# Kernel tuning notes

Hardware: AMD Instinct MI355X
Metric: run time of the kernel (lower is better)

## Reference

```python
import jax, jax.numpy as jnp
import numpy as np
import math

B, S, HID = 1, 4096, 2048
H, KVH, D = 32, 8, 64
N_REP = H // KVH  # 4


def _rope(x, cos, sin):
    # x: [B, h, S, D]; cos/sin: [S, D//2]
    x2 = x.reshape(*x.shape[:-1], D // 2, 2)
    x0, x1 = x2[..., 0], x2[..., 1]
    c = cos[None, None, :, :]
    s = sin[None, None, :, :]
    # complex multiply (x0 + i x1) * (c + i s)
    o0 = x0 * c - x1 * s
    o1 = x0 * s + x1 * c
    return jnp.stack([o0, o1], axis=-1).reshape(x.shape)


def setup_inputs() -> dict:
    key = jax.random.key(0)
    ks = jax.random.split(key, 6)
    hidden_states = jax.random.normal(ks[0], (B, S, 2 * HID), dtype=jnp.float32)
    scale = 0.02
    wq = jax.random.normal(ks[1], (H * D, 2 * HID), dtype=jnp.float32) * scale
    wk = jax.random.normal(ks[2], (KVH * D, 2 * HID), dtype=jnp.float32) * scale
    wv = jax.random.normal(ks[3], (KVH * D, 2 * HID), dtype=jnp.float32) * scale
    wo = jax.random.normal(ks[4], (HID, H * D), dtype=jnp.float32) * scale
    # standard RoPE frequencies (theta=10000), shape [S, D//2]
    inv_freq = 1.0 / (10000.0 ** (np.arange(0, D, 2, dtype=np.float32) / D))
    angles = np.arange(S, dtype=np.float32)[:, None] * inv_freq[None, :]
    freqs_cos = jnp.asarray(np.cos(angles), dtype=jnp.float32)
    freqs_sin = jnp.asarray(np.sin(angles), dtype=jnp.float32)
    return {"hidden_states": hidden_states, "wq": wq, "wk": wk, "wv": wv,
            "wo": wo, "freqs_cos": freqs_cos, "freqs_sin": freqs_sin}


def reference(hidden_states, wq, wk, wv, wo, freqs_cos, freqs_sin):
    bsz, q_len, _ = hidden_states.shape
    q = (hidden_states @ wq.T).reshape(bsz, q_len, H, D).transpose(0, 2, 1, 3)   # [B,H,S,D]
    k = (hidden_states @ wk.T).reshape(bsz, q_len, KVH, D).transpose(0, 2, 1, 3)  # [B,KVH,S,D]
    v = (hidden_states @ wv.T).reshape(bsz, q_len, KVH, D).transpose(0, 2, 1, 3)
    q = _rope(q, freqs_cos, freqs_sin)
    k = _rope(k, freqs_cos, freqs_sin)
    # GQA repeat_kv
    k = jnp.repeat(k, N_REP, axis=1)  # [B,H,S,D]
    v = jnp.repeat(v, N_REP, axis=1)
    scores = jnp.einsum('bhqd,bhkd->bhqk', q, k) / math.sqrt(D)  # [B,H,S,S]
    weights = jax.nn.softmax(scores.astype(jnp.float32), axis=-1).astype(q.dtype)
    attn = jnp.einsum('bhqk,bhkd->bhqd', weights, v)  # [B,H,S,D]
    attn = attn.transpose(0, 2, 1, 3).reshape(bsz, q_len, H * D)
    return attn @ wo.T  # [B,S,HID]
```

## Files before the change

kernel.cpp:

```cpp
#include <hip/hip_runtime.h>
#include <hip/hip_bf16.h>

typedef __attribute__((ext_vector_type(4))) float f32x4;
typedef __attribute__((ext_vector_type(8))) __bf16 bf16x8;
typedef __attribute__((ext_vector_type(8))) short short8;
typedef __attribute__((ext_vector_type(4))) short short4v;
typedef __attribute__((ext_vector_type(2))) unsigned int uint2v;

#define SEQ 4096
#define NQKV 3072

static __device__ __forceinline__ unsigned short f2bf(float x) {
  unsigned int u = __float_as_uint(x);
  u += 0x7fffu + ((u >> 16) & 1u);
  return (unsigned short)(u >> 16);
}
static __device__ __forceinline__ float bf2f(unsigned short b) {
  return __uint_as_float(((unsigned int)b) << 16);
}
static __device__ __forceinline__ unsigned int cvtpk_bf16(float lo, float hi) {
  unsigned int r;
  asm("v_cvt_pk_bf16_f32 %0, %1, %2" : "=v"(r) : "v"(lo), "v"(hi));
  return r;
}
static __device__ __forceinline__ float exp2_fast(float x) {
  float r;
  asm("v_exp_f32 %0, %1" : "=v"(r) : "v"(x));
  return r;
}

__global__ void cvt_f32_bf16(const float* __restrict__ src,
                             unsigned short* __restrict__ dst, int n4) {
  int i = blockIdx.x * blockDim.x + threadIdx.x;
  if (i >= n4) return;
  f32x4 v = ((const f32x4*)src)[i];
  short4v o;
#pragma unroll
  for (int j = 0; j < 4; ++j) o[j] = (short)f2bf(v[j]);
  ((short4v*)dst)[i] = o;
}

template <int BN, bool OUT_F32>
__global__ __launch_bounds__(512, 2) void gemm256(const unsigned short* __restrict__ A,
                                                  const unsigned short* __restrict__ Bt,
                                                  void* __restrict__ Cp,
                                                  int M, int N, int K) {
  constexpr int NJ = BN / 64;
  constexpr int TC = 16 + BN / 16;
  constexpr int SPW = (TC + 7) / 8;
  constexpr int DUP = 8 * SPW - TC;

  __shared__ unsigned short AbL[3][8192];
  __shared__ unsigned short BbL[3][BN * 32];

  const int t512 = threadIdx.x;
  const int l = t512 & 63;
  const int wid = t512 >> 6;
  const int wm = wid >> 2, wn = wid & 3;
  const int lr = l & 15, lg = l >> 4;
  const int m0 = blockIdx.y * 256, n0 = blockIdx.x * BN;

  const int lrow = l >> 2;
  const int scb = ((l & 3) << 4) ^ ((lrow & 3) << 4);

  const int rswz = (lr & 3) << 4;

  f32x4 acc[8][NJ];
#pragma unroll
  for (int i = 0; i < 8; ++i)
#pragma unroll
    for (int j = 0; j < NJ; ++j) acc[i][j] = (f32x4){0.f, 0.f, 0.f, 0.f};

  auto stage = [&](int buf, int t) {
    const int kt = t * 32;
#pragma unroll
    for (int s = 0; s < SPW; ++s) {
      int id = wid * SPW + s;
      if (DUP > 0 && id >= TC) id -= DUP;
      if (id < 16) {
        const char* src = (const char*)(A + (size_t)(m0 + id * 16 + lrow) * K + kt) + scb;
        __builtin_amdgcn_global_load_lds(
            (const __attribute__((address_space(1))) void*)src,
            (__attribute__((address_space(3))) void*)&AbL[buf][id * 512], 16, 0, 0);
      } else {
        const int b = id - 16;
        const char* src = (const char*)(Bt + (size_t)(n0 + b * 16 + lrow) * K + kt) + scb;
        __builtin_amdgcn_global_load_lds(
            (const __attribute__((address_space(1))) void*)src,
            (__attribute__((address_space(3))) void*)&BbL[buf][b * 512], 16, 0, 0);
      }
    }
  };

  const int NT = K / 32;

  stage(0, 0);
  stage(1, 1);
  if constexpr (SPW == 4) asm volatile("s_waitcnt vmcnt(4)" ::: "memory");
  else                    asm volatile("s_waitcnt vmcnt(3)" ::: "memory");
  __builtin_amdgcn_s_barrier();
  __builtin_amdgcn_sched_barrier(0);

  int cur = 0;
  for (int t = 0; t < NT; ++t) {
    int pf = cur + 2; if (pf >= 3) pf -= 3;
    if (t + 2 < NT) stage(pf, t + 2);

    const char* Ab0 = (const char*)&AbL[cur][0] + (size_t)(wm * 128 + lr) * 64;
    const char* Bb0 = (const char*)&BbL[cur][0] + (size_t)(wn * (BN / 4) + lr) * 64;
    bf16x8 af[8], bfv[NJ];
#pragma unroll
    for (int i = 0; i < 8; ++i)
      af[i] = *(const bf16x8*)(Ab0 + i * 1024 + ((lg * 16) ^ rswz));
#pragma unroll
    for (int j = 0; j < NJ; ++j)
      bfv[j] = *(const bf16x8*)(Bb0 + j * 1024 + ((lg * 16) ^ rswz));

    asm volatile("s_waitcnt lgkmcnt(0)" ::: "memory");
    __builtin_amdgcn_sched_barrier(0);

    __builtin_amdgcn_s_setprio(1);
#pragma unroll
    for (int i = 0; i < 8; ++i)
#pragma unroll
      for (int j = 0; j < NJ; ++j)
        acc[i][j] = __builtin_amdgcn_mfma_f32_16x16x32_bf16(af[i], bfv[j], acc[i][j], 0, 0, 0);
    __builtin_amdgcn_s_setprio(0);

    if (t + 2 < NT) {
      if constexpr (SPW == 4) asm volatile("s_waitcnt vmcnt(4)" ::: "memory");
      else                    asm volatile("s_waitcnt vmcnt(3)" ::: "memory");
    } else if (t + 1 < NT) {
      asm volatile("s_waitcnt vmcnt(0)" ::: "memory");
    }
    if (t + 1 < NT) {
      __builtin_amdgcn_s_barrier();
      __builtin_amdgcn_sched_barrier(0);
    }
    cur = (cur == 2) ? 0 : cur + 1;
  }

  const int row0 = m0 + wm * 128, col0 = n0 + wn * (BN / 4);
#pragma unroll
  for (int i = 0; i < 8; ++i) {
#pragma unroll
    for (int j = 0; j < NJ; ++j) {
      const int col = col0 + j * 16 + lr;
#pragma unroll
      for (int r = 0; r < 4; ++r) {
        const int row = row0 + i * 16 + lg * 4 + r;
        if (OUT_F32)
          ((float*)Cp)[(size_t)row * N + col] = acc[i][j][r];
        else
          ((unsigned short*)Cp)[(size_t)row * N + col] = f2bf(acc[i][j][r]);
      }
    }
  }
}

__global__ void rope_scale(unsigned short* __restrict__ qkv,
                           const float* __restrict__ fc,
                           const float* __restrict__ fs) {
  int idx = blockIdx.x * blockDim.x + threadIdx.x;
  int s = idx / 1280;
  int p = idx - s * 1280;
  bool isQ = (p < 1024);
  int col = isQ ? (p * 2) : (2048 + (p - 1024) * 2);
  int fi = (col >> 1) & 31;
  float c = fc[s * 32 + fi];
  float sn = fs[s * 32 + fi];
  unsigned short* ptr = qkv + (size_t)s * NQKV + col;
  float x0 = bf2f(ptr[0]);
  float x1 = bf2f(ptr[1]);
  float o0 = x0 * c - x1 * sn;
  float o1 = x0 * sn + x1 * c;
  float scl = isQ ? 0.1803368801111204f : 1.0f;
  ptr[0] = f2bf(o0 * scl);
  ptr[1] = f2bf(o1 * scl);
}

__global__ void v_transpose(const unsigned short* __restrict__ qkv,
                            unsigned short* __restrict__ Vt) {
  __shared__ unsigned short tile[64][72];
  const int kvh = blockIdx.x;
  const int st = blockIdx.y * 64;
  const int t = threadIdx.x;
  const int sl = t >> 2, d0 = (t & 3) * 16;
  const unsigned short* src = qkv + (size_t)(st + sl) * NQKV + 2560 + kvh * 64 + d0;
  *(bf16x8*)&tile[sl][d0] = *(const bf16x8*)src;
  *(bf16x8*)&tile[sl][d0 + 8] = *(const bf16x8*)(src + 8);
  __syncthreads();
  const int dl = t >> 2, s0 = (t & 3) * 16;
  unsigned short* dst = Vt + ((size_t)kvh * 64 + dl) * 4096 + st + s0;
#pragma unroll
  for (int j2 = 0; j2 < 2; ++j2) {
    short8 v;
#pragma unroll
    for (int j = 0; j < 8; ++j) v[j] = (short)tile[s0 + j2 * 8 + j][dl];
    *(short8*)(dst + j2 * 8) = v;
  }
}

__global__ __launch_bounds__(256, 4) void attn_fwd(const unsigned short* __restrict__ qkv,
                                                   const unsigned short* __restrict__ Vt,
                                                   unsigned short* __restrict__ attn) {
  __shared__ unsigned short Ks[2][4096];
  __shared__ unsigned short Vs[2][4096];
  __shared__ unsigned short Plds[4][1024];

  const int t = threadIdx.x;
  const int l = t & 63;
  const int w = t >> 6;
  const int lr = l & 15, lg = l >> 4;
  const int h = blockIdx.x;
  const int kvh = h >> 2;
  const int qbase = blockIdx.y * 128 + w * 32;

  const int chunk0 = w * 2;
  const int srow = l >> 3;
  const int scol = (l & 7) * 16;
  const int sorig = scol ^ ((srow & 7) << 4);
  const char* ksrc0 = (const char*)(qkv + 2048 + kvh * 64) +
                      (size_t)(chunk0 * 8 + srow) * (NQKV * 2) + sorig;
  const char* ksrc1 = ksrc0 + 8 * (NQKV * 2);
  const char* vsrc0 = (const char*)(Vt + (size_t)kvh * 64 * 4096) +
                      (size_t)(chunk0 * 8 + srow) * 8192 + sorig;
  const char* vsrc1 = vsrc0 + 8 * 8192;

  const int x = (lr & 7) << 4;
  const int x6 = x & 64, x45 = x & 48;
  const int offA = lr * 128 + x6 + ((lg * 16) ^ x45);
  const int offB = lr * 128 + (64 ^ x6) + ((lg * 16) ^ x45);

  const int pswz = ((lr & 7) << 4) ^ (w << 5);
  char* PldsB = (char*)Plds + w * 2048 + lr * 128;

  bf16x8 qf[2][2];
#pragma unroll
  for (int qi = 0; qi < 2; ++qi) {
    const unsigned short* qr = qkv + (size_t)(qbase + qi * 16 + lr) * NQKV + h * 64;
    qf[qi][0] = *(const bf16x8*)(qr + lg * 8);
    qf[qi][1] = *(const bf16x8*)(qr + 32 + lg * 8);
  }

  f32x4 ls4[2];
  f32x4 o[2][4];
#pragma unroll
  for (int qi = 0; qi < 2; ++qi) {
    ls4[qi] = (f32x4){0.f, 0.f, 0.f, 0.f};
#pragma unroll
    for (int c4 = 0; c4 < 4; ++c4) o[qi][c4] = (f32x4){0.f, 0.f, 0.f, 0.f};
  }

  auto stage = [&](int buf, int tile) {
    const size_t kadv = (size_t)tile * 64 * (NQKV * 2);
    const size_t vadv = (size_t)tile * 128;
    __builtin_amdgcn_global_load_lds(
        (const __attribute__((address_space(1))) void*)(ksrc0 + kadv),
        (__attribute__((address_space(3))) void*)&Ks[buf][chunk0 * 512], 16, 0, 0);
    __builtin_amdgcn_global_load_lds(
        (const __attribute__((address_space(1))) void*)(ksrc1 + kadv),
        (__attribute__((address_space(3))) void*)&Ks[buf][(chunk0 + 1) * 512], 16, 0, 0);
    __builtin_amdgcn_global_load_lds(
        (const __attribute__((address_space(1))) void*)(vsrc0 + vadv),
        (__attribute__((address_space(3))) void*)&Vs[buf][chunk0 * 512], 16, 0, 0);
    __builtin_amdgcn_global_load_lds(
        (const __attribute__((address_space(1))) void*)(vsrc1 + vadv),
        (__attribute__((address_space(3))) void*)&Vs[buf][(chunk0 + 1) * 512], 16, 0, 0);
  };

  stage(0, 0);
  asm volatile("s_waitcnt vmcnt(0)" ::: "memory");
  __syncthreads();

  const int NT = SEQ / 64;
  for (int tt = 0; tt < NT; ++tt) {
    const int buf = tt & 1;
    if (tt + 1 < NT) stage(buf ^ 1, tt + 1);

    const char* Ksb = (const char*)Ks[buf];
    const char* Vsb = (const char*)Vs[buf];

    f32x4 sc[2][4];
    __builtin_amdgcn_s_setprio(1);
#pragma unroll
    for (int sI = 0; sI < 4; ++sI) {
      bf16x8 kf0 = *(const bf16x8*)(Ksb + offA + sI * 2048);
      bf16x8 kf1 = *(const bf16x8*)(Ksb + offB + sI * 2048);
#pragma unroll
      for (int qi = 0; qi < 2; ++qi) {
        f32x4 c = (f32x4){0.f, 0.f, 0.f, 0.f};
        c = __builtin_amdgcn_mfma_f32_16x16x32_bf16(kf0, qf[qi][0], c, 0, 0, 0);
        c = __builtin_amdgcn_mfma_f32_16x16x32_bf16(kf1, qf[qi][1], c, 0, 0, 0);
        sc[qi][sI] = c;
      }
    }
    __builtin_amdgcn_s_setprio(0);

    bf16x8 pa[2][2];
#pragma unroll
    for (int qi = 0; qi < 2; ++qi) {
      float p[4][4];
#pragma unroll
      for (int sI = 0; sI < 4; ++sI)
#pragma unroll
        for (int r = 0; r < 4; ++r) p[sI][r] = exp2_fast(sc[qi][sI][r]);
#pragma unroll
      for (int sI = 0; sI < 4; ++sI)
#pragma unroll
        for (int r = 0; r < 4; ++r) ls4[qi][r] += p[sI][r];
#pragma unroll
      for (int sI = 0; sI < 4; ++sI) {
        uint2v pk;
        pk[0] = cvtpk_bf16(p[sI][0], p[sI][1]);
        pk[1] = cvtpk_bf16(p[sI][2], p[sI][3]);
        *(uint2v*)(PldsB + ((32 * sI + 8 * lg) ^ pswz)) = pk;
      }
      pa[qi][0] = *(const bf16x8*)(PldsB + ((16 * lg) ^ pswz));
      pa[qi][1] = *(const bf16x8*)(PldsB + ((64 + 16 * lg) ^ pswz));
    }

    __builtin_amdgcn_s_setprio(1);
#pragma unroll
    for (int c4 = 0; c4 < 4; ++c4) {
      bf16x8 v0 = *(const bf16x8*)(Vsb + offA + c4 * 2048);
      bf16x8 v1 = *(const bf16x8*)(Vsb + offB + c4 * 2048);
#pragma unroll
      for (int qi = 0; qi < 2; ++qi) {
        o[qi][c4] = __builtin_amdgcn_mfma_f32_16x16x32_bf16(pa[qi][0], v0, o[qi][c4], 0, 0, 0);
        o[qi][c4] = __builtin_amdgcn_mfma_f32_16x16x32_bf16(pa[qi][1], v1, o[qi][c4], 0, 0, 0);
      }
    }
    __builtin_amdgcn_s_setprio(0);

    asm volatile("s_waitcnt vmcnt(0)" ::: "memory");
    __syncthreads();
  }

#pragma unroll
  for (int qi = 0; qi < 2; ++qi) {
    float lsum = ls4[qi][0] + ls4[qi][1] + ls4[qi][2] + ls4[qi][3];
    lsum += __shfl_xor(lsum, 16, 64);
    lsum += __shfl_xor(lsum, 32, 64);
    float inv = 1.f / lsum;
    float invO[4];
#pragma unroll
    for (int r = 0; r < 4; ++r) invO[r] = __shfl(inv, 4 * lg + r, 64);
#pragma unroll
    for (int c4 = 0; c4 < 4; ++c4)
#pragma unroll
      for (int r = 0; r < 4; ++r) {
        attn[(size_t)(qbase + qi * 16 + 4 * lg + r) * 2048 + h * 64 + c4 * 16 + lr] =
            f2bf(o[qi][c4][r] * invO[r]);
      }
  }
}

extern "C" void kernel_launch(void* const* d_in, const int* in_sizes, int n_in,
                              void* d_out, int out_size, void* d_ws, size_t ws_size,
                              hipStream_t stream) {
  const float* hs = (const float*)d_in[0];
  const float* wq = (const float*)d_in[1];
  const float* wk = (const float*)d_in[2];
  const float* wv = (const float*)d_in[3];
  const float* wo = (const float*)d_in[4];
  const float* fc = (const float*)d_in[5];
  const float* fs = (const float*)d_in[6];
  float* out = (float*)d_out;

  char* ws = (char*)d_ws;
  unsigned short* Xb    = (unsigned short*)(ws);
  unsigned short* Wqkv  = (unsigned short*)(ws + (size_t)(32 << 20));
  unsigned short* Wob   = (unsigned short*)(ws + (size_t)(56 << 20));
  unsigned short* QKV   = (unsigned short*)(ws + (size_t)(64 << 20));
  unsigned short* attnb = Xb;
  unsigned short* Vtb   = (unsigned short*)(ws + (size_t)(16 << 20));

  cvt_f32_bf16<<<16384, 256, 0, stream>>>(hs, Xb, 4194304);
  cvt_f32_bf16<<<8192, 256, 0, stream>>>(wq, Wqkv, 2097152);
  cvt_f32_bf16<<<2048, 256, 0, stream>>>(wk, Wqkv + 8388608, 524288);
  cvt_f32_bf16<<<2048, 256, 0, stream>>>(wv, Wqkv + 10485760, 524288);
  cvt_f32_bf16<<<4096, 256, 0, stream>>>(wo, Wob, 1048576);

  gemm256<192, false><<<dim3(16, 16), 512, 0, stream>>>(Xb, Wqkv, QKV, 4096, 3072, 4096);

  v_transpose<<<dim3(8, 64), 256, 0, stream>>>(QKV, Vtb);
  rope_scale<<<20480, 256, 0, stream>>>(QKV, fc, fs);

  attn_fwd<<<dim3(32, 32), 256, 0, stream>>>(QKV, Vtb, attnb);

  gemm256<128, true><<<dim3(16, 16), 512, 0, stream>>>(attnb, Wob, out, 4096, 2048, 2048);
}
```

Before: 361.1 us.

## Fuse conversion launches, remap GEMM tiles, relax GEMM sync and occupancy

```diff
diff --git a/kernel.cpp b/kernel.cpp
--- a/kernel.cpp
+++ b/kernel.cpp
@@ -29,19 +29,29 @@
   return r;
 }
 
-__global__ void cvt_f32_bf16(const float* __restrict__ src,
-                             unsigned short* __restrict__ dst, int n4) {
+__global__ void cvt_all(const float* __restrict__ hs, const float* __restrict__ wq,
+                        const float* __restrict__ wk, const float* __restrict__ wv,
+                        const float* __restrict__ wo,
+                        unsigned short* __restrict__ Xb, unsigned short* __restrict__ Wqkv,
+                        unsigned short* __restrict__ Wob) {
   int i = blockIdx.x * blockDim.x + threadIdx.x;
-  if (i >= n4) return;
-  f32x4 v = ((const f32x4*)src)[i];
+  const float* src;
+  unsigned short* dst;
+  int off;
+  if (i < 4194304)      { src = hs; dst = Xb;              off = i; }
+  else if (i < 6291456) { src = wq; dst = Wqkv;            off = i - 4194304; }
+  else if (i < 6815744) { src = wk; dst = Wqkv + 8388608;  off = i - 6291456; }
+  else if (i < 7340032) { src = wv; dst = Wqkv + 10485760; off = i - 6815744; }
+  else                  { src = wo; dst = Wob;             off = i - 7340032; }
+  f32x4 v = ((const f32x4*)src)[off];
   short4v o;
 #pragma unroll
   for (int j = 0; j < 4; ++j) o[j] = (short)f2bf(v[j]);
-  ((short4v*)dst)[i] = o;
+  ((short4v*)dst)[off] = o;
 }
 
 template <int BN, bool OUT_F32>
-__global__ __launch_bounds__(512, 2) void gemm256(const unsigned short* __restrict__ A,
+__global__ __launch_bounds__(512, 1) void gemm256(const unsigned short* __restrict__ A,
                                                   const unsigned short* __restrict__ Bt,
                                                   void* __restrict__ Cp,
                                                   int M, int N, int K) {
@@ -58,7 +68,10 @@
   const int wid = t512 >> 6;
   const int wm = wid >> 2, wn = wid & 3;
   const int lr = l & 15, lg = l >> 4;
-  const int m0 = blockIdx.y * 256, n0 = blockIdx.x * BN;
+
+  const int bid = blockIdx.y * 16 + blockIdx.x;
+  const int nid = (bid & 7) * 32 + (bid >> 3);
+  const int m0 = (nid >> 4) * 256, n0 = (nid & 15) * BN;
 
   const int lrow = l >> 2;
   const int scb = ((l & 3) << 4) ^ ((lrow & 3) << 4);
@@ -99,7 +112,7 @@
   if constexpr (SPW == 4) asm volatile("s_waitcnt vmcnt(4)" ::: "memory");
   else                    asm volatile("s_waitcnt vmcnt(3)" ::: "memory");
   __builtin_amdgcn_s_barrier();
-  __builtin_amdgcn_sched_barrier(0);
+  asm volatile("" ::: "memory");
 
   int cur = 0;
   for (int t = 0; t < NT; ++t) {
@@ -115,9 +128,6 @@
 #pragma unroll
     for (int j = 0; j < NJ; ++j)
       bfv[j] = *(const bf16x8*)(Bb0 + j * 1024 + ((lg * 16) ^ rswz));
-
-    asm volatile("s_waitcnt lgkmcnt(0)" ::: "memory");
-    __builtin_amdgcn_sched_barrier(0);
 
     __builtin_amdgcn_s_setprio(1);
 #pragma unroll
@@ -134,8 +144,9 @@
       asm volatile("s_waitcnt vmcnt(0)" ::: "memory");
     }
     if (t + 1 < NT) {
+      asm volatile("s_waitcnt lgkmcnt(0)" ::: "memory");
       __builtin_amdgcn_s_barrier();
-      __builtin_amdgcn_sched_barrier(0);
+      asm volatile("" ::: "memory");
     }
     cur = (cur == 2) ? 0 : cur + 1;
   }
@@ -376,11 +387,7 @@
   unsigned short* attnb = Xb;
   unsigned short* Vtb   = (unsigned short*)(ws + (size_t)(16 << 20));
 
-  cvt_f32_bf16<<<16384, 256, 0, stream>>>(hs, Xb, 4194304);
-  cvt_f32_bf16<<<8192, 256, 0, stream>>>(wq, Wqkv, 2097152);
-  cvt_f32_bf16<<<2048, 256, 0, stream>>>(wk, Wqkv + 8388608, 524288);
-  cvt_f32_bf16<<<2048, 256, 0, stream>>>(wv, Wqkv + 10485760, 524288);
-  cvt_f32_bf16<<<4096, 256, 0, stream>>>(wo, Wob, 1048576);
+  cvt_all<<<32768, 256, 0, stream>>>(hs, wq, wk, wv, wo, Xb, Wqkv, Wob);
 
   gemm256<192, false><<<dim3(16, 16), 512, 0, stream>>>(Xb, Wqkv, QKV, 4096, 3072, 4096);
 
```

Result: no change. 354.2 us (-1.9%).
